# Kernel optimization log

Measured on AMD Instinct MI355X. Metric: run time of the kernel, lower is better.

Reference implementation:

```python
import jax, jax.numpy as jnp
import numpy as np

EPS = 1e-6
H = 16
CHUNK = 128

def _fmap(x):
    # elu(x) + 1 positive feature map
    return jax.nn.elu(x) + 1.0

def _causal_lin_attn(Qf, Kf, V, eps):
    # Math-identical chunkwise form of the cumsum causal linear attention.
    B, Hh, N, D = Qf.shape
    Dv = V.shape[-1]
    nc = N // CHUNK
    qs = jnp.moveaxis(Qf.reshape(B, Hh, nc, CHUNK, D), 2, 0)
    ks = jnp.moveaxis(Kf.reshape(B, Hh, nc, CHUNK, D), 2, 0)
    vs = jnp.moveaxis(V.reshape(B, Hh, nc, CHUNK, Dv), 2, 0)
    mask = jnp.tril(jnp.ones((CHUNK, CHUNK), dtype=bool))  # inclusive causal within chunk
    S0 = jnp.zeros((B, Hh, D, Dv), Qf.dtype)
    z0 = jnp.zeros((B, Hh, D), Qf.dtype)

    def step(carry, xs):
        S, z = carry
        q, k, v = xs  # (B,H,C,D), (B,H,C,D), (B,H,C,Dv)
        A = jnp.einsum('bhqd,bhkd->bhqk', q, k)
        A = jnp.where(mask, A, 0.0)
        num = jnp.einsum('bhqd,bhdv->bhqv', q, S) + jnp.einsum('bhqk,bhkv->bhqv', A, v)
        den = jnp.einsum('bhqd,bhd->bhq', q, z) + A.sum(-1)
        out = num / (den[..., None] + eps)
        S = S + jnp.einsum('bhkd,bhkv->bhdv', k, v)
        z = z + k.sum(2)
        return (S, z), out

    _, out = jax.lax.scan(step, (S0, z0), (qs, ks, vs))
    return jnp.moveaxis(out, 0, 2).reshape(B, Hh, N, Dv)

def _mhla(Q, K, V, Wq, Wk, Wv, Wo, causal):
    B, N, E = Q.shape
    D = E // H
    q = (Q @ Wq.T).reshape(B, N, H, D).transpose(0, 2, 1, 3)  # (B,H,N,D)
    k = (K @ Wk.T).reshape(B, N, H, D).transpose(0, 2, 1, 3)
    v = (V @ Wv.T).reshape(B, N, H, D).transpose(0, 2, 1, 3)
    Qf, Kf = _fmap(q), _fmap(k)
    if causal:
        out = _causal_lin_attn(Qf, Kf, v, EPS)
    else:
        KV = jnp.einsum('bhnd,bhnv->bhdv', Kf, v)
        ksum = Kf.sum(2)
        num = jnp.einsum('bhnd,bhdv->bhnv', Qf, KV)
        den = jnp.einsum('bhnd,bhd->bhn', Qf, ksum)[..., None]
        out = num / (den + EPS)
    out = out.transpose(0, 2, 1, 3).reshape(B, N, E)
    return out @ Wo.T

def setup_inputs():
    key = jax.random.key(0)
    ks = jax.random.split(key, 7)
    B, N, E = 2, 2048, 1024

    def xavier(k, shape):
        lim = (6.0 / (shape[0] + shape[1])) ** 0.5
        return jax.random.uniform(k, shape, jnp.float32, -lim, lim)

    return {
        'Q': jax.random.normal(ks[0], (B, N, E), jnp.float32),
        'K': jax.random.normal(ks[1], (B, N, E), jnp.float32),
        'V': jax.random.normal(ks[2], (B, N, E), jnp.float32),
        'Wq': xavier(ks[3], (E, E)),
        'Wk': xavier(ks[4], (E, E)),
        'Wv': xavier(ks[5], (E, E)),
        'Wo': xavier(ks[6], (E, E)),
        'causal': 1,
    }

def reference(Q, K, V, Wq, Wk, Wv, Wo, causal):
    return _mhla(Q, K, V, Wq, Wk, Wv, Wo, causal)
```

## Files before the change

### kernel.cpp

```cpp
#include <hip/hip_runtime.h>
#include <hip/hip_bf16.h>
#include <stdint.h>

#define B_   2
#define N_   2048
#define E_   1024
#define H_   16
#define D_   64
#define CH_  128
#define NC_  16
#define BH_  32
#define M_   4096
#define K_   1024
#define EPS_F 1e-6f

typedef __attribute__((ext_vector_type(8))) __bf16 bf16x8;
typedef __attribute__((ext_vector_type(4))) float  f32x4;

static __device__ __forceinline__ f32x4 mfma16(bf16x8 a, bf16x8 b, f32x4 c) {
  return __builtin_amdgcn_mfma_f32_16x16x32_bf16(a, b, c, 0, 0, 0);
}

static __device__ __forceinline__ unsigned short f2bf(float f) {
  union { float fv; unsigned int u; } x; x.fv = f;
  unsigned int r = x.u + 0x7FFFu + ((x.u >> 16) & 1u);
  return (unsigned short)(r >> 16);
}
static __device__ __forceinline__ float fmap(float x) {
  return x > 0.f ? (x + 1.f) : __expf(x);
}
static __device__ __forceinline__ void gload16(const void* g, void* l) {
  __builtin_amdgcn_global_load_lds(
      (const __attribute__((address_space(1))) void*)g,
      (__attribute__((address_space(3))) void*)l, 16, 0, 0);
}

__global__ __launch_bounds__(256)
void conv_kernel(const float* __restrict__ Q, const float* __restrict__ Kx,
                 const float* __restrict__ V, const float* __restrict__ Wq,
                 const float* __restrict__ Wk, const float* __restrict__ Wv,
                 const float* __restrict__ Wo,
                 unsigned short* __restrict__ Xb, unsigned short* __restrict__ Wb) {
  int gid = blockIdx.x * 256 + threadIdx.x;
  int idx = gid * 4;
  const float* src; unsigned short* dst; int off;
  if (idx < (3 << 22)) {
    int which = idx >> 22;
    off = idx & ((1 << 22) - 1);
    src = (which == 0) ? Q : (which == 1) ? Kx : V;
    dst = Xb + ((size_t)which << 22);
  } else {
    int j = idx - (3 << 22);
    int which = j >> 20;
    off = j & ((1 << 20) - 1);
    src = (which == 0) ? Wq : (which == 1) ? Wk : (which == 2) ? Wv : Wo;
    dst = Wb + ((size_t)which << 20);
  }
  float4 v = *(const float4*)(src + off);
  ushort4 o;
  o.x = f2bf(v.x); o.y = f2bf(v.y); o.z = f2bf(v.z); o.w = f2bf(v.w);
  *(ushort4*)(dst + off) = o;
}

template<int MODE>
__global__ __launch_bounds__(256)
void gemm_kernel(const unsigned short* __restrict__ Aall,
                 const unsigned short* __restrict__ Wall,
                 unsigned short* __restrict__ qf,
                 unsigned short* __restrict__ kf,
                 unsigned short* __restrict__ kt,
                 unsigned short* __restrict__ vt,
                 float* __restrict__ outf) {
  constexpr int BM = (MODE == 0) ? 128 : 64;
  constexpr int WM = BM / 32;
  constexpr int RA = BM / 32;
  constexpr int NWG = (MODE == 0) ? 768 : 512;
  __shared__ __align__(16) unsigned short As[BM * 64];
  __shared__ __align__(16) unsigned short Bs[128 * 64];

  const int wg = (blockIdx.x & 7) * (NWG >> 3) + (blockIdx.x >> 3);
  const int nb = wg & 7;
  const int mb = (MODE == 0) ? ((wg >> 3) & 31) : (wg >> 3);
  const int z  = (MODE == 0) ? (wg >> 8) : 3;

  const unsigned short* Ag = Aall + ((MODE == 0) ? ((size_t)z << 22) : 0);
  const unsigned short* Bg = Wall + ((size_t)z << 20);
  const int tid = threadIdx.x;
  const int w = tid >> 6, l = tid & 63;
  const int wm = w >> 1, wn = w & 1;
  const int fl = l & 15, fh = l >> 4;

  const int srow  = w * 8 + (l >> 3);
  const int sslot = (l & 7) ^ (l >> 3);
  const unsigned short* gA = Ag + (size_t)(mb * BM + srow) * K_ + sslot * 8;
  const unsigned short* gB = Bg + (size_t)(nb * 128 + srow) * K_ + sslot * 8;

  const int rswz = (fl & 7) << 3;

  f32x4 acc[WM][4] = {};

  for (int k0 = 0; k0 < K_; k0 += 64) {
    __syncthreads();
#pragma unroll
    for (int r = 0; r < RA; r++)
      gload16(gA + (size_t)r * 32 * K_ + k0, As + (r * 32 + w * 8) * 64);
#pragma unroll
    for (int r = 0; r < 4; r++)
      gload16(gB + (size_t)r * 32 * K_ + k0, Bs + (r * 32 + w * 8) * 64);
    __syncthreads();
#pragma unroll
    for (int kk = 0; kk < 2; kk++) {
      bf16x8 av[WM], bv[4];
#pragma unroll
      for (int i = 0; i < WM; i++)
        av[i] = *(const bf16x8*)(As + (wm * (BM / 2) + i * 16 + fl) * 64
                                    + ((kk * 32 + fh * 8) ^ rswz));
#pragma unroll
      for (int j = 0; j < 4; j++)
        bv[j] = *(const bf16x8*)(Bs + (wn * 64 + j * 16 + fl) * 64
                                    + ((kk * 32 + fh * 8) ^ rswz));
#pragma unroll
      for (int i = 0; i < WM; i++)
#pragma unroll
        for (int j = 0; j < 4; j++)
          acc[i][j] = mfma16(av[i], bv[j], acc[i][j]);
    }
  }

#pragma unroll
  for (int i = 0; i < WM; i++)
#pragma unroll
    for (int j = 0; j < 4; j++)
#pragma unroll
      for (int r = 0; r < 4; r++) {
        int m = mb * BM + wm * (BM / 2) + i * 16 + fh * 4 + r;
        int e = nb * 128 + wn * 64 + j * 16 + fl;
        float v = acc[i][j][r];
        if (MODE == 1) {
          outf[(size_t)m * E_ + e] = v;
        } else {
          int b = m >> 11, n = m & (N_ - 1), h = e >> 6, d = e & 63;
          int bh = b * H_ + h;
          if (z == 0) {
            qf[((size_t)bh * N_ + n) * D_ + d] = f2bf(fmap(v));
          } else if (z == 1) {
            unsigned short s = f2bf(fmap(v));
            kf[((size_t)bh * N_ + n) * D_ + d] = s;
            kt[((size_t)bh * D_ + d) * N_ + n] = s;
          } else {
            vt[((size_t)bh * D_ + d) * N_ + n] = f2bf(v);
          }
        }
      }
}

__global__ __launch_bounds__(64)
void chunkkv_kernel(const unsigned short* __restrict__ kt,
                    const unsigned short* __restrict__ vt,
                    float* __restrict__ Sc, float* __restrict__ zc) {
  const int bh = blockIdx.x, c = blockIdx.y;
  const int l = threadIdx.x;
  const int fl = l & 15, fh = l >> 4;
  const int n0 = c * CH_;
  const unsigned short* ktb = kt + (size_t)bh * D_ * N_;
  const unsigned short* vtb = vt + (size_t)bh * D_ * N_;
  f32x4 acc[4][4] = {};
#pragma unroll
  for (int ks = 0; ks < 4; ks++) {
    bf16x8 av[4], bv[4];
#pragma unroll
    for (int i = 0; i < 4; i++)
      av[i] = *(const bf16x8*)(vtb + (size_t)(i * 16 + fl) * N_ + n0 + ks * 32 + fh * 8);
#pragma unroll
    for (int j = 0; j < 4; j++)
      bv[j] = *(const bf16x8*)(ktb + (size_t)(j * 16 + fl) * N_ + n0 + ks * 32 + fh * 8);
#pragma unroll
    for (int i = 0; i < 4; i++)
#pragma unroll
      for (int j = 0; j < 4; j++)
        acc[i][j] = mfma16(av[i], bv[j], acc[i][j]);
  }
  float* Scb = Sc + ((size_t)(bh * NC_ + c) << 12);
#pragma unroll
  for (int i = 0; i < 4; i++)
#pragma unroll
    for (int j = 0; j < 4; j++)
#pragma unroll
      for (int r = 0; r < 4; r++)
        Scb[(i * 16 + fh * 4 + r) * 64 + j * 16 + fl] = acc[i][j][r];
  float s = 0.f;
  const unsigned short* kr = ktb + (size_t)l * N_ + n0;
#pragma unroll
  for (int t = 0; t < 16; t++) {
    bf16x8 v8 = *(const bf16x8*)(kr + t * 8);
#pragma unroll
    for (int e = 0; e < 8; e++) s += (float)v8[e];
  }
  zc[(bh * NC_ + c) * 64 + l] = s;
}

__global__ __launch_bounds__(256)
void attn_kernel(const unsigned short* __restrict__ qf,
                 const unsigned short* __restrict__ kf,
                 const unsigned short* __restrict__ vt,
                 const float* __restrict__ Sc,
                 const float* __restrict__ zc,
                 unsigned short* __restrict__ AO) {
  __shared__ __align__(16) unsigned short A_lds[128 * 136];
  __shared__ __align__(16) unsigned short St_lds[64 * 64];
  __shared__ float zx_lds[64];
  __shared__ float den_s[128][2];
  const int c = blockIdx.x, bh = blockIdx.y;
  const int tid = threadIdx.x, w = tid >> 6, l = tid & 63;
  const int fl = l & 15, fh = l >> 4;
  const int n0 = c * CH_;
  const unsigned short* qfb = qf + ((size_t)bh * N_ + n0) * D_;
  const unsigned short* kfb = kf + ((size_t)bh * N_ + n0) * D_;
  const unsigned short* vtb = vt + (size_t)bh * D_ * N_;

  f32x4 accA[2][8] = {};
#pragma unroll
  for (int ks = 0; ks < 2; ks++) {
    bf16x8 av[2], bv[8];
#pragma unroll
    for (int i = 0; i < 2; i++)
      av[i] = *(const bf16x8*)(qfb + (size_t)(w * 32 + i * 16 + fl) * D_ + ks * 32 + fh * 8);
#pragma unroll
    for (int j = 0; j < 8; j++)
      bv[j] = *(const bf16x8*)(kfb + (size_t)(j * 16 + fl) * D_ + ks * 32 + fh * 8);
#pragma unroll
    for (int i = 0; i < 2; i++)
#pragma unroll
      for (int j = 0; j < 8; j++)
        accA[i][j] = mfma16(av[i], bv[j], accA[i][j]);
  }
#pragma unroll
  for (int i = 0; i < 2; i++)
#pragma unroll
    for (int j = 0; j < 8; j++)
#pragma unroll
      for (int r = 0; r < 4; r++) {
        int qrow = w * 32 + i * 16 + fh * 4 + r;
        int kcol = j * 16 + fl;
        float v = (kcol <= qrow) ? accA[i][j][r] : 0.f;
        A_lds[qrow * 136 + kcol] = f2bf(v);
      }

  {
    float s[16];
#pragma unroll
    for (int j = 0; j < 16; j++) s[j] = 0.f;
    for (int c2 = 0; c2 < c; c2++) {
      const float* b = Sc + (((size_t)(bh * NC_ + c2)) << 12);
#pragma unroll
      for (int j = 0; j < 16; j++) s[j] += b[tid + j * 256];
    }
#pragma unroll
    for (int j = 0; j < 16; j++) {
      int fi = tid + j * 256;
      int rw = (fi >> 6) & 7;
      St_lds[fi ^ (rw << 3)] = f2bf(s[j]);
    }
    if (tid < 64) {
      float zs = 0.f;
      for (int c2 = 0; c2 < c; c2++) zs += zc[(bh * NC_ + c2) * 64 + tid];
      zx_lds[tid] = zs;
    }
  }
  __syncthreads();

  {
    int row = tid >> 1, h2 = tid & 1;
    float dq = 0.f;
    const unsigned short* qr = qfb + (size_t)row * D_;
#pragma unroll
    for (int t = 0; t < 4; t++) {
      bf16x8 q8 = *(const bf16x8*)(qr + (h2 * 4 + t) * 8);
#pragma unroll
      for (int e = 0; e < 8; e++) dq += (float)q8[e] * zx_lds[(h2 * 4 + t) * 8 + e];
    }
#pragma unroll
    for (int t = 0; t < 8; t++) {
      bf16x8 a8 = *(const bf16x8*)(A_lds + row * 136 + (h2 * 8 + t) * 8);
#pragma unroll
      for (int e = 0; e < 8; e++) dq += (float)a8[e];
    }
    den_s[row][h2] = dq;
  }
  __syncthreads();

  const int rswz = (fl & 7) << 3;
  f32x4 accO[2][4] = {};
#pragma unroll
  for (int ks = 0; ks < 2; ks++) {
    bf16x8 av[2], bv[4];
#pragma unroll
    for (int i = 0; i < 2; i++)
      av[i] = *(const bf16x8*)(qfb + (size_t)(w * 32 + i * 16 + fl) * D_ + ks * 32 + fh * 8);
#pragma unroll
    for (int j = 0; j < 4; j++)
      bv[j] = *(const bf16x8*)(St_lds + (j * 16 + fl) * 64 + ((ks * 32 + fh * 8) ^ rswz));
#pragma unroll
    for (int i = 0; i < 2; i++)
#pragma unroll
      for (int j = 0; j < 4; j++)
        accO[i][j] = mfma16(av[i], bv[j], accO[i][j]);
  }
#pragma unroll
  for (int ks = 0; ks < 4; ks++) {
    bf16x8 av[2], bv[4];
#pragma unroll
    for (int i = 0; i < 2; i++)
      av[i] = *(const bf16x8*)(A_lds + (w * 32 + i * 16 + fl) * 136 + ks * 32 + fh * 8);
#pragma unroll
    for (int j = 0; j < 4; j++)
      bv[j] = *(const bf16x8*)(vtb + (size_t)(j * 16 + fl) * N_ + n0 + ks * 32 + fh * 8);
#pragma unroll
    for (int i = 0; i < 2; i++)
#pragma unroll
      for (int j = 0; j < 4; j++)
        accO[i][j] = mfma16(av[i], bv[j], accO[i][j]);
  }

  const int b = bh >> 4, h = bh & 15;
#pragma unroll
  for (int i = 0; i < 2; i++)
#pragma unroll
    for (int j = 0; j < 4; j++)
#pragma unroll
      for (int r = 0; r < 4; r++) {
        int qrow = w * 32 + i * 16 + fh * 4 + r;
        int dv = j * 16 + fl;
        float den = den_s[qrow][0] + den_s[qrow][1] + EPS_F;
        float o = accO[i][j][r] / den;
        AO[((size_t)(b * N_ + n0 + qrow)) * E_ + h * 64 + dv] = f2bf(o);
      }
}

extern "C" void kernel_launch(void* const* d_in, const int* in_sizes, int n_in,
                              void* d_out, int out_size, void* d_ws, size_t ws_size,
                              hipStream_t stream) {
  const float* Q  = (const float*)d_in[0];
  const float* Kx = (const float*)d_in[1];
  const float* V  = (const float*)d_in[2];
  const float* Wq = (const float*)d_in[3];
  const float* Wk = (const float*)d_in[4];
  const float* Wv = (const float*)d_in[5];
  const float* Wo = (const float*)d_in[6];

  char* p = (char*)d_ws;
  unsigned short* Xb = (unsigned short*)p; p += (size_t)3 * M_ * K_ * 2;
  unsigned short* Wb = (unsigned short*)p; p += (size_t)4 * E_ * E_ * 2;
  unsigned short* qf = (unsigned short*)p; p += (size_t)BH_ * N_ * D_ * 2;
  unsigned short* kf = (unsigned short*)p; p += (size_t)BH_ * N_ * D_ * 2;
  unsigned short* kt = (unsigned short*)p; p += (size_t)BH_ * N_ * D_ * 2;
  unsigned short* vt = (unsigned short*)p; p += (size_t)BH_ * N_ * D_ * 2;
  float*          Sc = (float*)p;          p += (size_t)BH_ * NC_ * D_ * D_ * 4;
  float*          zc = (float*)p;          p += (size_t)BH_ * NC_ * D_ * 4;
  unsigned short* AO = (unsigned short*)p; p += (size_t)M_ * E_ * 2;

  conv_kernel<<<dim3(16384), dim3(256), 0, stream>>>(Q, Kx, V, Wq, Wk, Wv, Wo, Xb, Wb);
  gemm_kernel<0><<<dim3(768), dim3(256), 0, stream>>>(Xb, Wb, qf, kf, kt, vt, nullptr);
  chunkkv_kernel<<<dim3(32, 16), dim3(64), 0, stream>>>(kt, vt, Sc, zc);
  attn_kernel<<<dim3(16, 32), dim3(256), 0, stream>>>(qf, kf, vt, Sc, zc, AO);
  gemm_kernel<1><<<dim3(512), dim3(256), 0, stream>>>(AO, Wb, nullptr, nullptr,
                                                      nullptr, nullptr, (float*)d_out);
}
```

Before: 218.3 us.

## Load GEMM MFMA operands directly from global memory with register double-buffering

The GEMM kernel no longer stages A and B tiles in LDS through global_load_lds with two barriers per k-step. Each wave now loads its MFMA fragments straight from global memory into registers, double-buffered so the next k-slice loads while the current one is multiplied. This removes LDS traffic and the __syncthreads barriers. In exchange, wave pairs that share rows now load the same data redundantly from global/L2, and the per-lane loads are only 16-byte strided accesses instead of coalesced tile loads.

```diff
diff --git a/kernel.cpp b/kernel.cpp
--- a/kernel.cpp
+++ b/kernel.cpp
@@ -28,11 +28,6 @@
 }
 static __device__ __forceinline__ float fmap(float x) {
   return x > 0.f ? (x + 1.f) : __expf(x);
-}
-static __device__ __forceinline__ void gload16(const void* g, void* l) {
-  __builtin_amdgcn_global_load_lds(
-      (const __attribute__((address_space(1))) void*)g,
-      (__attribute__((address_space(3))) void*)l, 16, 0, 0);
 }
 
 __global__ __launch_bounds__(256)
@@ -73,10 +68,7 @@
                  float* __restrict__ outf) {
   constexpr int BM = (MODE == 0) ? 128 : 64;
   constexpr int WM = BM / 32;
-  constexpr int RA = BM / 32;
   constexpr int NWG = (MODE == 0) ? 768 : 512;
-  __shared__ __align__(16) unsigned short As[BM * 64];
-  __shared__ __align__(16) unsigned short Bs[128 * 64];
 
   const int wg = (blockIdx.x & 7) * (NWG >> 3) + (blockIdx.x >> 3);
   const int nb = wg & 7;
@@ -90,42 +82,38 @@
   const int wm = w >> 1, wn = w & 1;
   const int fl = l & 15, fh = l >> 4;
 
-  const int srow  = w * 8 + (l >> 3);
-  const int sslot = (l & 7) ^ (l >> 3);
-  const unsigned short* gA = Ag + (size_t)(mb * BM + srow) * K_ + sslot * 8;
-  const unsigned short* gB = Bg + (size_t)(nb * 128 + srow) * K_ + sslot * 8;
-
-  const int rswz = (fl & 7) << 3;
+  const unsigned short* pA = Ag + (size_t)(mb * BM + wm * (BM / 2) + fl) * K_ + fh * 8;
+  const unsigned short* pB = Bg + (size_t)(nb * 128 + wn * 64 + fl) * K_ + fh * 8;
 
   f32x4 acc[WM][4] = {};
-
-  for (int k0 = 0; k0 < K_; k0 += 64) {
-    __syncthreads();
-#pragma unroll
-    for (int r = 0; r < RA; r++)
-      gload16(gA + (size_t)r * 32 * K_ + k0, As + (r * 32 + w * 8) * 64);
-#pragma unroll
-    for (int r = 0; r < 4; r++)
-      gload16(gB + (size_t)r * 32 * K_ + k0, Bs + (r * 32 + w * 8) * 64);
-    __syncthreads();
-#pragma unroll
-    for (int kk = 0; kk < 2; kk++) {
-      bf16x8 av[WM], bv[4];
-#pragma unroll
-      for (int i = 0; i < WM; i++)
-        av[i] = *(const bf16x8*)(As + (wm * (BM / 2) + i * 16 + fl) * 64
-                                    + ((kk * 32 + fh * 8) ^ rswz));
+  bf16x8 a0[WM], b0[4], a1[WM], b1[4];
+
+  auto LD = [&](bf16x8* ab, bf16x8* bb, int kk) {
+#pragma unroll
+    for (int i = 0; i < WM; i++)
+      ab[i] = *(const bf16x8*)(pA + (size_t)(i * 16) * K_ + kk);
+#pragma unroll
+    for (int j = 0; j < 4; j++)
+      bb[j] = *(const bf16x8*)(pB + (size_t)(j * 16) * K_ + kk);
+  };
+  auto FM = [&](bf16x8* ab, bf16x8* bb) {
+#pragma unroll
+    for (int i = 0; i < WM; i++)
 #pragma unroll
       for (int j = 0; j < 4; j++)
-        bv[j] = *(const bf16x8*)(Bs + (wn * 64 + j * 16 + fl) * 64
-                                    + ((kk * 32 + fh * 8) ^ rswz));
-#pragma unroll
-      for (int i = 0; i < WM; i++)
-#pragma unroll
-        for (int j = 0; j < 4; j++)
-          acc[i][j] = mfma16(av[i], bv[j], acc[i][j]);
-    }
-  }
+        acc[i][j] = mfma16(ab[i], bb[j], acc[i][j]);
+  };
+
+  LD(a0, b0, 0);
+  for (int k0 = 0; k0 < K_ - 64; k0 += 64) {
+    LD(a1, b1, k0 + 32);
+    FM(a0, b0);
+    LD(a0, b0, k0 + 64);
+    FM(a1, b1);
+  }
+  LD(a1, b1, K_ - 32);
+  FM(a0, b0);
+  FM(a1, b1);
 
 #pragma unroll
   for (int i = 0; i < WM; i++)
```

Result: slower. 299.7 us (+37.3%).

## Split-K output GEMM with bf16 partials and reduce; shrink K-tile to 32

Applied to the files above, without the earlier changes.

The output projection GEMM is split along K into two slices, doubling its workgroup count to 1024. Each slice writes bf16 partial results into a reused workspace, and a new reduce kernel sums them into the fp32 output. The shared K-tile also shrinks from 64 to 32 with a new LDS swizzle, which affects both GEMM modes. This trades an extra kernel launch, extra memory traffic and bf16 rounding of partials for more parallelism on the small GEMM, while the smaller K-tile doubles the number of barriers per K step.

```diff
diff --git a/kernel.cpp b/kernel.cpp
--- a/kernel.cpp
+++ b/kernel.cpp
@@ -15,6 +15,7 @@
 #define EPS_F 1e-6f
 
 typedef __attribute__((ext_vector_type(8))) __bf16 bf16x8;
+typedef __attribute__((ext_vector_type(8))) unsigned short u16x8;
 typedef __attribute__((ext_vector_type(4))) float  f32x4;
 
 static __device__ __forceinline__ f32x4 mfma16(bf16x8 a, bf16x8 b, f32x4 c) {
@@ -25,6 +26,10 @@
   union { float fv; unsigned int u; } x; x.fv = f;
   unsigned int r = x.u + 0x7FFFu + ((x.u >> 16) & 1u);
   return (unsigned short)(r >> 16);
+}
+static __device__ __forceinline__ float bf2f(unsigned short s) {
+  union { unsigned int u; float f; } x; x.u = ((unsigned int)s) << 16;
+  return x.f;
 }
 static __device__ __forceinline__ float fmap(float x) {
   return x > 0.f ? (x + 1.f) : __expf(x);
@@ -70,18 +75,22 @@
                  unsigned short* __restrict__ kf,
                  unsigned short* __restrict__ kt,
                  unsigned short* __restrict__ vt,
-                 float* __restrict__ outf) {
-  constexpr int BM = (MODE == 0) ? 128 : 64;
-  constexpr int WM = BM / 32;
-  constexpr int RA = BM / 32;
-  constexpr int NWG = (MODE == 0) ? 768 : 512;
-  __shared__ __align__(16) unsigned short As[BM * 64];
-  __shared__ __align__(16) unsigned short Bs[128 * 64];
+                 unsigned short* __restrict__ partf) {
+  constexpr int BM   = (MODE == 0) ? 128 : 64;
+  constexpr int WM   = BM / 32;
+  constexpr int NWG  = (MODE == 0) ? 768 : 1024;
+  constexpr int KLEN = (MODE == 0) ? K_ : 512;
+  __shared__ __align__(16) unsigned short As[BM * 32];
+  __shared__ __align__(16) unsigned short Bs[128 * 32];
 
   const int wg = (blockIdx.x & 7) * (NWG >> 3) + (blockIdx.x >> 3);
-  const int nb = wg & 7;
-  const int mb = (MODE == 0) ? ((wg >> 3) & 31) : (wg >> 3);
-  const int z  = (MODE == 0) ? (wg >> 8) : 3;
+  int nb, mb, z, kbase, slice;
+  if constexpr (MODE == 0) {
+    nb = wg & 7; mb = (wg >> 3) & 31; z = wg >> 8; kbase = 0; slice = 0;
+  } else {
+    slice = wg >> 9; int rem = wg & 511;
+    nb = rem & 7; mb = rem >> 3; z = 3; kbase = slice * 512;
+  }
 
   const unsigned short* Ag = Aall + ((MODE == 0) ? ((size_t)z << 22) : 0);
   const unsigned short* Bg = Wall + ((size_t)z << 20);
@@ -89,42 +98,37 @@
   const int w = tid >> 6, l = tid & 63;
   const int wm = w >> 1, wn = w & 1;
   const int fl = l & 15, fh = l >> 4;
-
-  const int srow  = w * 8 + (l >> 3);
-  const int sslot = (l & 7) ^ (l >> 3);
-  const unsigned short* gA = Ag + (size_t)(mb * BM + srow) * K_ + sslot * 8;
-  const unsigned short* gB = Bg + (size_t)(nb * 128 + srow) * K_ + sslot * 8;
-
-  const int rswz = (fl & 7) << 3;
+  const int lrow = l >> 2;
+  const int swz = (l & 3) ^ ((l >> 3) & 3);
+
+  const unsigned short* gA = Ag + (size_t)(mb * BM + w * (BM / 4) + lrow) * K_ + swz * 8;
+  const unsigned short* gB = Bg + (size_t)(nb * 128 + w * 32 + lrow) * K_ + swz * 8;
+  unsigned short* lA = As + w * (BM / 4) * 32;
+  unsigned short* lB = Bs + w * 1024;
+
+  const int rs = (fh ^ ((fl >> 1) & 3)) * 8;
 
   f32x4 acc[WM][4] = {};
 
-  for (int k0 = 0; k0 < K_; k0 += 64) {
+  for (int k0 = kbase; k0 < kbase + KLEN; k0 += 32) {
     __syncthreads();
-#pragma unroll
-    for (int r = 0; r < RA; r++)
-      gload16(gA + (size_t)r * 32 * K_ + k0, As + (r * 32 + w * 8) * 64);
-#pragma unroll
-    for (int r = 0; r < 4; r++)
-      gload16(gB + (size_t)r * 32 * K_ + k0, Bs + (r * 32 + w * 8) * 64);
+    gload16(gA + k0, lA);
+    if constexpr (MODE == 0) gload16(gA + k0 + 16 * K_, lA + 512);
+    gload16(gB + k0, lB);
+    gload16(gB + k0 + 16 * K_, lB + 512);
     __syncthreads();
-#pragma unroll
-    for (int kk = 0; kk < 2; kk++) {
-      bf16x8 av[WM], bv[4];
-#pragma unroll
-      for (int i = 0; i < WM; i++)
-        av[i] = *(const bf16x8*)(As + (wm * (BM / 2) + i * 16 + fl) * 64
-                                    + ((kk * 32 + fh * 8) ^ rswz));
+    bf16x8 av[WM], bv[4];
+#pragma unroll
+    for (int i = 0; i < WM; i++)
+      av[i] = *(const bf16x8*)(As + (wm * (BM / 2) + i * 16 + fl) * 32 + rs);
+#pragma unroll
+    for (int j = 0; j < 4; j++)
+      bv[j] = *(const bf16x8*)(Bs + (wn * 64 + j * 16 + fl) * 32 + rs);
+#pragma unroll
+    for (int i = 0; i < WM; i++)
 #pragma unroll
       for (int j = 0; j < 4; j++)
-        bv[j] = *(const bf16x8*)(Bs + (wn * 64 + j * 16 + fl) * 64
-                                    + ((kk * 32 + fh * 8) ^ rswz));
-#pragma unroll
-      for (int i = 0; i < WM; i++)
-#pragma unroll
-        for (int j = 0; j < 4; j++)
-          acc[i][j] = mfma16(av[i], bv[j], acc[i][j]);
-    }
+        acc[i][j] = mfma16(av[i], bv[j], acc[i][j]);
   }
 
 #pragma unroll
@@ -137,7 +141,7 @@
         int e = nb * 128 + wn * 64 + j * 16 + fl;
         float v = acc[i][j][r];
         if (MODE == 1) {
-          outf[(size_t)m * E_ + e] = v;
+          partf[((size_t)slice << 22) + (size_t)m * E_ + e] = f2bf(v);
         } else {
           int b = m >> 11, n = m & (N_ - 1), h = e >> 6, d = e & 63;
           int bh = b * H_ + h;
@@ -152,6 +156,20 @@
           }
         }
       }
+}
+
+__global__ __launch_bounds__(256)
+void reduce_kernel(const unsigned short* __restrict__ P, float* __restrict__ out) {
+  int i = (blockIdx.x * 256 + threadIdx.x) * 8;
+  u16x8 a = *(const u16x8*)(P + i);
+  u16x8 b = *(const u16x8*)(P + (1 << 22) + i);
+  float4 o0, o1;
+  o0.x = bf2f(a[0]) + bf2f(b[0]);  o0.y = bf2f(a[1]) + bf2f(b[1]);
+  o0.z = bf2f(a[2]) + bf2f(b[2]);  o0.w = bf2f(a[3]) + bf2f(b[3]);
+  o1.x = bf2f(a[4]) + bf2f(b[4]);  o1.y = bf2f(a[5]) + bf2f(b[5]);
+  o1.z = bf2f(a[6]) + bf2f(b[6]);  o1.w = bf2f(a[7]) + bf2f(b[7]);
+  *(float4*)(out + i)     = o0;
+  *(float4*)(out + i + 4) = o1;
 }
 
 __global__ __launch_bounds__(64)
@@ -358,11 +376,13 @@
   float*          Sc = (float*)p;          p += (size_t)BH_ * NC_ * D_ * D_ * 4;
   float*          zc = (float*)p;          p += (size_t)BH_ * NC_ * D_ * 4;
   unsigned short* AO = (unsigned short*)p; p += (size_t)M_ * E_ * 2;
+  unsigned short* Pf = Xb;
 
   conv_kernel<<<dim3(16384), dim3(256), 0, stream>>>(Q, Kx, V, Wq, Wk, Wv, Wo, Xb, Wb);
   gemm_kernel<0><<<dim3(768), dim3(256), 0, stream>>>(Xb, Wb, qf, kf, kt, vt, nullptr);
   chunkkv_kernel<<<dim3(32, 16), dim3(64), 0, stream>>>(kt, vt, Sc, zc);
   attn_kernel<<<dim3(16, 32), dim3(256), 0, stream>>>(qf, kf, vt, Sc, zc, AO);
-  gemm_kernel<1><<<dim3(512), dim3(256), 0, stream>>>(AO, Wb, nullptr, nullptr,
-                                                      nullptr, nullptr, (float*)d_out);
-}
+  gemm_kernel<1><<<dim3(1024), dim3(256), 0, stream>>>(AO, Wb, nullptr, nullptr,
+                                                       nullptr, nullptr, Pf);
+  reduce_kernel<<<dim3(2048), dim3(256), 0, stream>>>(Pf, (float*)d_out);
+}
```

New measurement: 220.2 us. About the same (+0.9%).
